# Kernel optimization log

Measured on AMD Instinct MI355X. Metric: run time of the kernel, lower is better.

Reference implementation:

```python
import jax, jax.numpy as jnp
import numpy as np

E = 1024      # embedding_size
H = 16        # num_heads
D = E // H    # head dim


def setup_inputs() -> dict:
    key = jax.random.key(0)
    k1, k2, k3, k4, k5 = jax.random.split(key, 5)
    x = jax.random.normal(k1, (4, 2048, E), dtype=jnp.float32)
    # nn.Linear(E, 3E): weight [3E, E], bias [3E]
    w_qkv = jax.random.normal(k2, (3 * E, E), dtype=jnp.float32) * (1.0 / np.sqrt(E))
    b_qkv = jax.random.normal(k3, (3 * E,), dtype=jnp.float32) * 0.02
    # nn.Linear(E, E)
    w_proj = jax.random.normal(k4, (E, E), dtype=jnp.float32) * (1.0 / np.sqrt(E))
    b_proj = jax.random.normal(k5, (E,), dtype=jnp.float32) * 0.02
    return {"x": x, "w_qkv": w_qkv, "b_qkv": b_qkv, "w_proj": w_proj, "b_proj": b_proj}


def reference(x, w_qkv, b_qkv, w_proj, b_proj):
    b, n, _ = x.shape
    qkv = x @ w_qkv.T + b_qkv                       # [b, n, 3E]
    # rearrange 'b n (h d qkv) -> qkv b h n d' : last dim grouped as (h, d, 3)
    qkv = qkv.reshape(b, n, H, D, 3)
    qkv = jnp.transpose(qkv, (4, 0, 2, 1, 3))        # [3, b, h, n, d]
    q, k, v = qkv[0], qkv[1], qkv[2]
    scale = 1.0 / np.sqrt(E / H)
    energy = jnp.einsum('bhqd,bhkd->bhqk', q, k) * scale
    attn = jax.nn.softmax(energy, axis=-1)
    out = jnp.einsum('bhqk,bhkd->bhqd', attn, v)     # [b, h, n, d]
    out = jnp.transpose(out, (0, 2, 1, 3)).reshape(b, n, E)
    return out @ w_proj.T + b_proj
```

## Files before the change

### kernel.cpp

```cpp
#include <hip/hip_runtime.h>
#include <hip/hip_fp16.h>

namespace {

constexpr int B = 4;
constexpr int N = 2048;
constexpr int E = 1024;
constexpr int H = 16;
constexpr int D = 64;
constexpr int M = B * N;

typedef __attribute__((ext_vector_type(8))) short bf16x8;
typedef __attribute__((ext_vector_type(8))) _Float16 f16x8;
typedef __attribute__((ext_vector_type(4))) float f32x4;

__device__ inline ushort bf16_rne(float f) {
  unsigned u = __float_as_uint(f);
  return (ushort)((u + 0x7FFFu + ((u >> 16) & 1u)) >> 16);
}
__device__ inline void split2(float f, ushort& hi, ushort& lo) {
  unsigned u = __float_as_uint(f);
  hi = (ushort)(u >> 16);
  lo = bf16_rne(f - __uint_as_float(u & 0xFFFF0000u));
}

__global__ __launch_bounds__(256) void split_kernel(
    const float* __restrict__ in, ushort* __restrict__ hi,
    ushort* __restrict__ lo, int n4) {
  int i = blockIdx.x * blockDim.x + threadIdx.x;
  const int stride = gridDim.x * blockDim.x;
  for (; i < n4; i += stride) {
    const float4 f = ((const float4*)in)[i];
    ushort4 h, l;
    split2(f.x, h.x, l.x);
    split2(f.y, h.y, l.y);
    split2(f.z, h.z, l.z);
    split2(f.w, h.w, l.w);
    ((ushort4*)hi)[i] = h;
    ((ushort4*)lo)[i] = l;
  }
}

template <int MODE>
__global__ __launch_bounds__(256) void gemm_x3(
    const ushort* __restrict__ Ahg, const ushort* __restrict__ Alg,
    const ushort* __restrict__ Bhg, const ushort* __restrict__ Blg,
    const float* __restrict__ bias, ushort* __restrict__ qh,
    ushort* __restrict__ ql, ushort* __restrict__ kh, ushort* __restrict__ kl,
    ushort* __restrict__ vt, float* __restrict__ outp) {
  __shared__ ushort LAh[4096], LAl[4096], LBh[4096], LBl[4096];
  const int tid = threadIdx.x;
  const int l = tid & 63, wid = tid >> 6;
  const int wr = wid >> 1, wc = wid & 1;
  const int lr = l & 15, kg = l >> 4;
  const int m0 = blockIdx.x * 128, n0 = blockIdx.y * 128;

  f32x4 acc[4][4];
#pragma unroll
  for (int i = 0; i < 4; ++i)
#pragma unroll
    for (int j = 0; j < 4; ++j) acc[i][j] = (f32x4){0.f, 0.f, 0.f, 0.f};

  for (int k0 = 0; k0 < E; k0 += 32) {
    const ushort* gAh = Ahg + (size_t)m0 * E + k0;
    const ushort* gAl = Alg + (size_t)m0 * E + k0;
    const ushort* gBh = Bhg + (size_t)n0 * E + k0;
    const ushort* gBl = Blg + (size_t)n0 * E + k0;
    __syncthreads();
    auto stage = [&](const ushort* gp, ushort* lp, int half) {
      const int c = half * 256 + tid;
      __builtin_amdgcn_global_load_lds(
          (__attribute__((address_space(1))) void*)(gp + (size_t)(c >> 2) * E +
                                                    (c & 3) * 8),
          (__attribute__((address_space(3))) void*)(lp +
                                                    (half * 256 + (tid & ~63)) * 8),
          16, 0, 0);
    };
    stage(gAh, LAh, 0); stage(gAh, LAh, 1);
    stage(gAl, LAl, 0); stage(gAl, LAl, 1);
    stage(gBh, LBh, 0); stage(gBh, LBh, 1);
    stage(gBl, LBl, 0); stage(gBl, LBl, 1);
    __syncthreads();

    bf16x8 aH[4], aL[4], bH[4], bL[4];
#pragma unroll
    for (int rb = 0; rb < 4; ++rb) {
      const int off = (wr * 64 + rb * 16 + lr) * 32 + kg * 8;
      aH[rb] = *(const bf16x8*)(LAh + off);
      aL[rb] = *(const bf16x8*)(LAl + off);
    }
#pragma unroll
    for (int cb = 0; cb < 4; ++cb) {
      const int off = (wc * 64 + cb * 16 + lr) * 32 + kg * 8;
      bH[cb] = *(const bf16x8*)(LBh + off);
      bL[cb] = *(const bf16x8*)(LBl + off);
    }
#pragma unroll
    for (int rb = 0; rb < 4; ++rb)
#pragma unroll
      for (int cb = 0; cb < 4; ++cb) {
        acc[rb][cb] = __builtin_amdgcn_mfma_f32_16x16x32_bf16(
            aH[rb], bH[cb], acc[rb][cb], 0, 0, 0);
        acc[rb][cb] = __builtin_amdgcn_mfma_f32_16x16x32_bf16(
            aH[rb], bL[cb], acc[rb][cb], 0, 0, 0);
        acc[rb][cb] = __builtin_amdgcn_mfma_f32_16x16x32_bf16(
            aL[rb], bH[cb], acc[rb][cb], 0, 0, 0);
      }
  }

#pragma unroll
  for (int cb = 0; cb < 4; ++cb) {
    const int col = n0 + wc * 64 + cb * 16 + lr;
    const float bv = bias[col];
    if (MODE == 0) {
      const int h = col / 192;
      const int rem = col - h * 192;
      const int dd = rem / 3;
      const int s = rem - dd * 3;
#pragma unroll
      for (int rb = 0; rb < 4; ++rb)
#pragma unroll
        for (int r = 0; r < 4; ++r) {
          const int m = m0 + wr * 64 + rb * 16 + kg * 4 + r;
          const int bb = m >> 11, nn = m & (N - 1);
          float v = acc[rb][cb][r] + bv;
          if (s == 0) {
            v *= 0.125f;
            ushort hi, lo;
            split2(v, hi, lo);
            const size_t idx = (((size_t)bb * H + h) * N + nn) * D + dd;
            qh[idx] = hi; ql[idx] = lo;
          } else if (s == 1) {
            ushort hi, lo;
            split2(v, hi, lo);
            const size_t idx = (((size_t)bb * H + h) * N + nn) * D + dd;
            kh[idx] = hi; kl[idx] = lo;
          } else {
            ((_Float16*)vt)[(((size_t)bb * H + h) * D + dd) * N + nn] =
                (_Float16)v;
          }
        }
    } else {
#pragma unroll
      for (int rb = 0; rb < 4; ++rb)
#pragma unroll
        for (int r = 0; r < 4; ++r) {
          const int m = m0 + wr * 64 + rb * 16 + kg * 4 + r;
          outp[(size_t)m * E + col] = acc[rb][cb][r] + bv;
        }
    }
  }
}

__global__ __launch_bounds__(256, 2) void attn_mfma(
    const ushort* __restrict__ Qh, const ushort* __restrict__ Ql,
    const ushort* __restrict__ Kh, const ushort* __restrict__ Kl,
    const ushort* __restrict__ Vt, ushort* __restrict__ Aoh,
    ushort* __restrict__ Aol) {
  __shared__ ushort KhL[4096], KlL[4096], VtL[4096], PsL[4][4096];
  const int tid = threadIdx.x;
  const int l = tid & 63, w = tid >> 6;
  const int lr = l & 15, g = l >> 4;
  const int bh = blockIdx.x, bb = bh >> 4, hh = bh & 15;
  const int q0 = blockIdx.y * 256 + w * 64;

  bf16x8 qfh[4][2], qfl[4][2];
#pragma unroll
  for (int rb = 0; rb < 4; ++rb)
#pragma unroll
    for (int ks = 0; ks < 2; ++ks) {
      const size_t off =
          ((size_t)bh * N + q0 + rb * 16 + lr) * D + ks * 32 + g * 8;
      qfh[rb][ks] = *(const bf16x8*)(Qh + off);
      qfl[rb][ks] = *(const bf16x8*)(Ql + off);
    }

  f32x4 o[4][4];
  float m_[4][4], l_[4][4];
#pragma unroll
  for (int rb = 0; rb < 4; ++rb)
#pragma unroll
    for (int r = 0; r < 4; ++r) {
      m_[rb][r] = -1e30f;
      l_[rb][r] = 0.f;
      o[rb][r] = (f32x4){0.f, 0.f, 0.f, 0.f};
    }

  ushort* Pw = &PsL[w][0];

  for (int kt = 0; kt < N / 64; ++kt) {
    __syncthreads();
#pragma unroll
    for (int bch = 0; bch < 2; ++bch) {
      const int s = bch * 256 + tid;
      const int r = s >> 3, c = s & 7;
      const int cc = (c ^ (r & 7)) * 8;
      const int dst = (bch * 256 + (tid & ~63)) * 8;
      const size_t ko = ((size_t)bh * N + kt * 64 + r) * D + cc;
      const size_t vo = ((size_t)bh * D + r) * N + kt * 64 + cc;
      __builtin_amdgcn_global_load_lds(
          (__attribute__((address_space(1))) void*)(Kh + ko),
          (__attribute__((address_space(3))) void*)(KhL + dst), 16, 0, 0);
      __builtin_amdgcn_global_load_lds(
          (__attribute__((address_space(1))) void*)(Kl + ko),
          (__attribute__((address_space(3))) void*)(KlL + dst), 16, 0, 0);
      __builtin_amdgcn_global_load_lds(
          (__attribute__((address_space(1))) void*)(Vt + vo),
          (__attribute__((address_space(3))) void*)(VtL + dst), 16, 0, 0);
    }
    __syncthreads();

    f32x4 s4[4][4];
#pragma unroll
    for (int rb = 0; rb < 4; ++rb)
#pragma unroll
      for (int cb = 0; cb < 4; ++cb) s4[rb][cb] = (f32x4){0.f, 0.f, 0.f, 0.f};
#pragma unroll
    for (int ks = 0; ks < 2; ++ks) {
      bf16x8 kfh[4], kfl[4];
#pragma unroll
      for (int cb = 0; cb < 4; ++cb) {
        const int sl = (cb * 16 + lr) * 8 + ((ks * 4 + g) ^ (lr & 7));
        kfh[cb] = *(const bf16x8*)(KhL + sl * 8);
        kfl[cb] = *(const bf16x8*)(KlL + sl * 8);
      }
#pragma unroll
      for (int rb = 0; rb < 4; ++rb)
#pragma unroll
        for (int cb = 0; cb < 4; ++cb) {
          s4[rb][cb] = __builtin_amdgcn_mfma_f32_16x16x32_bf16(
              qfh[rb][ks], kfh[cb], s4[rb][cb], 0, 0, 0);
          s4[rb][cb] = __builtin_amdgcn_mfma_f32_16x16x32_bf16(
              qfh[rb][ks], kfl[cb], s4[rb][cb], 0, 0, 0);
          s4[rb][cb] = __builtin_amdgcn_mfma_f32_16x16x32_bf16(
              qfl[rb][ks], kfh[cb], s4[rb][cb], 0, 0, 0);
        }
    }

#pragma unroll
    for (int rb = 0; rb < 4; ++rb)
#pragma unroll
      for (int r = 0; r < 4; ++r) {
        float mx = fmaxf(fmaxf(s4[rb][0][r], s4[rb][1][r]),
                         fmaxf(s4[rb][2][r], s4[rb][3][r]));
        mx = fmaxf(mx, __shfl_xor(mx, 1, 16));
        mx = fmaxf(mx, __shfl_xor(mx, 2, 16));
        mx = fmaxf(mx, __shfl_xor(mx, 4, 16));
        mx = fmaxf(mx, __shfl_xor(mx, 8, 16));
        const float mn = fmaxf(m_[rb][r], mx);
        const float fac = __expf(m_[rb][r] - mn);
        m_[rb][r] = mn;
        float sum = 0.f;
#pragma unroll
        for (int cb = 0; cb < 4; ++cb) {
          const float p = __expf(s4[rb][cb][r] - mn);
          s4[rb][cb][r] = p;
          sum += p;
        }
        sum += __shfl_xor(sum, 1, 16);
        sum += __shfl_xor(sum, 2, 16);
        sum += __shfl_xor(sum, 4, 16);
        sum += __shfl_xor(sum, 8, 16);
        l_[rb][r] = l_[rb][r] * fac + sum;
#pragma unroll
        for (int cb = 0; cb < 4; ++cb) o[rb][cb][r] *= fac;
        const int row = rb * 16 + g * 4 + r;
#pragma unroll
        for (int cb = 0; cb < 4; ++cb) {
          const int idx = (row * 64 + cb * 16 + lr) ^ ((row & 7) << 3);
          ((_Float16*)Pw)[idx] = (_Float16)s4[rb][cb][r];
        }
      }

#pragma unroll
    for (int ks = 0; ks < 2; ++ks) {
      f16x8 pf[4], vf[4];
#pragma unroll
      for (int rb = 0; rb < 4; ++rb) {
        const int sl = (rb * 16 + lr) * 8 + ((ks * 4 + g) ^ (lr & 7));
        pf[rb] = *(const f16x8*)(Pw + sl * 8);
      }
#pragma unroll
      for (int cb = 0; cb < 4; ++cb) {
        const int sl = (cb * 16 + lr) * 8 + ((ks * 4 + g) ^ (lr & 7));
        vf[cb] = *(const f16x8*)(VtL + sl * 8);
      }
#pragma unroll
      for (int rb = 0; rb < 4; ++rb)
#pragma unroll
        for (int cb = 0; cb < 4; ++cb)
          o[rb][cb] = __builtin_amdgcn_mfma_f32_16x16x32_f16(
              pf[rb], vf[cb], o[rb][cb], 0, 0, 0);
    }
  }

#pragma unroll
  for (int rb = 0; rb < 4; ++rb)
#pragma unroll
    for (int r = 0; r < 4; ++r) {
      const float inv = 1.f / l_[rb][r];
      const int n = q0 + rb * 16 + g * 4 + r;
      const size_t base = ((size_t)bb * N + n) * E + hh * D;
#pragma unroll
      for (int cb = 0; cb < 4; ++cb) {
        ushort hi, lo;
        split2(o[rb][cb][r] * inv, hi, lo);
        Aoh[base + cb * 16 + lr] = hi;
        Aol[base + cb * 16 + lr] = lo;
      }
    }
}

}

extern "C" void kernel_launch(void* const* d_in, const int* in_sizes, int n_in,
                              void* d_out, int out_size, void* d_ws,
                              size_t ws_size, hipStream_t stream) {
  (void)in_sizes; (void)n_in; (void)out_size; (void)ws_size;
  const float* x      = (const float*)d_in[0];
  const float* w_qkv  = (const float*)d_in[1];
  const float* b_qkv  = (const float*)d_in[2];
  const float* w_proj = (const float*)d_in[3];
  const float* b_proj = (const float*)d_in[4];
  float* out = (float*)d_out;

  constexpr size_t MB = 1ull << 20;
  char* w = (char*)d_ws;
  ushort* xh  = (ushort*)(w + 0 * MB);
  ushort* xl  = (ushort*)(w + 16 * MB);
  ushort* wqh = (ushort*)(w + 32 * MB);
  ushort* wql = (ushort*)(w + 38 * MB);
  ushort* wph = (ushort*)(w + 44 * MB);
  ushort* wpl = (ushort*)(w + 46 * MB);
  ushort* Aoh = (ushort*)(w + 48 * MB);
  ushort* Aol = (ushort*)(w + 64 * MB);
  ushort* Qh  = (ushort*)(w + 80 * MB);
  ushort* Ql  = (ushort*)(w + 96 * MB);
  ushort* Kh  = (ushort*)(w + 112 * MB);
  ushort* Kl  = (ushort*)(w + 128 * MB);
  ushort* Vt  = (ushort*)(w + 144 * MB);

  split_kernel<<<2048, 256, 0, stream>>>(x, xh, xl, (M * E) / 4);
  split_kernel<<<1024, 256, 0, stream>>>(w_qkv, wqh, wql, (3 * E * E) / 4);
  split_kernel<<<512, 256, 0, stream>>>(w_proj, wph, wpl, (E * E) / 4);

  gemm_x3<0><<<dim3(M / 128, 3 * E / 128), 256, 0, stream>>>(
      xh, xl, wqh, wql, b_qkv, Qh, Ql, Kh, Kl, Vt, nullptr);

  attn_mfma<<<dim3(B * H, N / 256), 256, 0, stream>>>(Qh, Ql, Kh, Kl, Vt, Aoh,
                                                      Aol);

  gemm_x3<1><<<dim3(M / 128, E / 128), 256, 0, stream>>>(
      Aoh, Aol, wph, wpl, b_proj, nullptr, nullptr, nullptr, nullptr, nullptr,
      out);
}
```

Measured before the change: 1.128 ms.

## Double-buffer attention K/V tiles, remap grid, and vectorize V-transpose stores

The attention kernel now double-buffers the K-hi, K-lo and V tiles in LDS. It prefetches the next key tile with direct global-to-LDS loads while computing on the current one, using manual vmcnt waits and barriers, and raises wave priority around the MFMA sections. The launch becomes a 1-D grid with a remapped block-to-head order, intended to improve L2 locality across XCDs. The QKV GEMM epilogue writes the transposed V as packed 4-wide fp16 stores instead of scalar stores. The extra LDS buffers increase shared memory use, which may reduce occupancy.

```diff
diff --git a/kernel.cpp b/kernel.cpp
--- a/kernel.cpp
+++ b/kernel.cpp
@@ -12,6 +12,7 @@
 
 typedef __attribute__((ext_vector_type(8))) short bf16x8;
 typedef __attribute__((ext_vector_type(8))) _Float16 f16x8;
+typedef __attribute__((ext_vector_type(4))) _Float16 f16x4;
 typedef __attribute__((ext_vector_type(4))) float f32x4;
 
 __device__ inline ushort bf16_rne(float f) {
@@ -117,29 +118,38 @@
       const int rem = col - h * 192;
       const int dd = rem / 3;
       const int s = rem - dd * 3;
-#pragma unroll
-      for (int rb = 0; rb < 4; ++rb)
-#pragma unroll
-        for (int r = 0; r < 4; ++r) {
-          const int m = m0 + wr * 64 + rb * 16 + kg * 4 + r;
+      if (s == 2) {
+#pragma unroll
+        for (int rb = 0; rb < 4; ++rb) {
+          const int m = m0 + wr * 64 + rb * 16 + kg * 4;
           const int bb = m >> 11, nn = m & (N - 1);
-          float v = acc[rb][cb][r] + bv;
-          if (s == 0) {
-            v *= 0.125f;
+          f16x4 pk;
+#pragma unroll
+          for (int r = 0; r < 4; ++r)
+            pk[r] = (_Float16)(acc[rb][cb][r] + bv);
+          *(f16x4*)((_Float16*)vt + (((size_t)bb * H + h) * D + dd) * N + nn) =
+              pk;
+        }
+      } else {
+#pragma unroll
+        for (int rb = 0; rb < 4; ++rb)
+#pragma unroll
+          for (int r = 0; r < 4; ++r) {
+            const int m = m0 + wr * 64 + rb * 16 + kg * 4 + r;
+            const int bb = m >> 11, nn = m & (N - 1);
+            float v = acc[rb][cb][r] + bv;
             ushort hi, lo;
-            split2(v, hi, lo);
             const size_t idx = (((size_t)bb * H + h) * N + nn) * D + dd;
-            qh[idx] = hi; ql[idx] = lo;
-          } else if (s == 1) {
-            ushort hi, lo;
-            split2(v, hi, lo);
-            const size_t idx = (((size_t)bb * H + h) * N + nn) * D + dd;
-            kh[idx] = hi; kl[idx] = lo;
-          } else {
-            ((_Float16*)vt)[(((size_t)bb * H + h) * D + dd) * N + nn] =
-                (_Float16)v;
+            if (s == 0) {
+              v *= 0.125f;
+              split2(v, hi, lo);
+              qh[idx] = hi; ql[idx] = lo;
+            } else {
+              split2(v, hi, lo);
+              kh[idx] = hi; kl[idx] = lo;
+            }
           }
-        }
+      }
     } else {
 #pragma unroll
       for (int rb = 0; rb < 4; ++rb)
@@ -157,12 +167,15 @@
     const ushort* __restrict__ Kh, const ushort* __restrict__ Kl,
     const ushort* __restrict__ Vt, ushort* __restrict__ Aoh,
     ushort* __restrict__ Aol) {
-  __shared__ ushort KhL[4096], KlL[4096], VtL[4096], PsL[4][4096];
+  __shared__ ushort KhL[2][4096], KlL[2][4096], VtL[2][4096], PsL[4][4096];
   const int tid = threadIdx.x;
   const int l = tid & 63, w = tid >> 6;
   const int lr = l & 15, g = l >> 4;
-  const int bh = blockIdx.x, bb = bh >> 4, hh = bh & 15;
-  const int q0 = blockIdx.y * 256 + w * 64;
+  const int id = blockIdx.x;
+  const int bh = (id & 7) * 8 + ((id >> 3) & 7);
+  const int qt = id >> 6;
+  const int bb = bh >> 4, hh = bh & 15;
+  const int q0 = qt * 256 + w * 64;
 
   bf16x8 qfh[4][2], qfl[4][2];
 #pragma unroll
@@ -188,41 +201,58 @@
 
   ushort* Pw = &PsL[w][0];
 
-  for (int kt = 0; kt < N / 64; ++kt) {
-    __syncthreads();
+  auto stage = [&](int buf, int kt) {
 #pragma unroll
     for (int bch = 0; bch < 2; ++bch) {
       const int s = bch * 256 + tid;
       const int r = s >> 3, c = s & 7;
       const int cc = (c ^ (r & 7)) * 8;
-      const int dst = (bch * 256 + (tid & ~63)) * 8;
+      const int dst = buf * 4096 + (bch * 256 + (tid & ~63)) * 8;
       const size_t ko = ((size_t)bh * N + kt * 64 + r) * D + cc;
       const size_t vo = ((size_t)bh * D + r) * N + kt * 64 + cc;
       __builtin_amdgcn_global_load_lds(
           (__attribute__((address_space(1))) void*)(Kh + ko),
-          (__attribute__((address_space(3))) void*)(KhL + dst), 16, 0, 0);
+          (__attribute__((address_space(3))) void*)(&KhL[0][0] + dst), 16, 0, 0);
       __builtin_amdgcn_global_load_lds(
           (__attribute__((address_space(1))) void*)(Kl + ko),
-          (__attribute__((address_space(3))) void*)(KlL + dst), 16, 0, 0);
+          (__attribute__((address_space(3))) void*)(&KlL[0][0] + dst), 16, 0, 0);
       __builtin_amdgcn_global_load_lds(
           (__attribute__((address_space(1))) void*)(Vt + vo),
-          (__attribute__((address_space(3))) void*)(VtL + dst), 16, 0, 0);
-    }
-    __syncthreads();
+          (__attribute__((address_space(3))) void*)(&VtL[0][0] + dst), 16, 0, 0);
+    }
+  };
+
+  constexpr int NT = N / 64;
+  stage(0, 0);
+  int cur = 0;
+
+  for (int kt = 0; kt < NT; ++kt) {
+    if (kt + 1 < NT) {
+      stage(cur ^ 1, kt + 1);
+      asm volatile("s_waitcnt vmcnt(6)" ::: "memory");
+    } else {
+      asm volatile("s_waitcnt vmcnt(0)" ::: "memory");
+    }
+    __builtin_amdgcn_s_barrier();
+
+    const ushort* KhC = &KhL[cur][0];
+    const ushort* KlC = &KlL[cur][0];
+    const ushort* VtC = &VtL[cur][0];
 
     f32x4 s4[4][4];
 #pragma unroll
     for (int rb = 0; rb < 4; ++rb)
 #pragma unroll
       for (int cb = 0; cb < 4; ++cb) s4[rb][cb] = (f32x4){0.f, 0.f, 0.f, 0.f};
+    __builtin_amdgcn_s_setprio(1);
 #pragma unroll
     for (int ks = 0; ks < 2; ++ks) {
       bf16x8 kfh[4], kfl[4];
 #pragma unroll
       for (int cb = 0; cb < 4; ++cb) {
         const int sl = (cb * 16 + lr) * 8 + ((ks * 4 + g) ^ (lr & 7));
-        kfh[cb] = *(const bf16x8*)(KhL + sl * 8);
-        kfl[cb] = *(const bf16x8*)(KlL + sl * 8);
+        kfh[cb] = *(const bf16x8*)(KhC + sl * 8);
+        kfl[cb] = *(const bf16x8*)(KlC + sl * 8);
       }
 #pragma unroll
       for (int rb = 0; rb < 4; ++rb)
@@ -236,6 +266,7 @@
               qfl[rb][ks], kfh[cb], s4[rb][cb], 0, 0, 0);
         }
     }
+    __builtin_amdgcn_s_setprio(0);
 
 #pragma unroll
     for (int rb = 0; rb < 4; ++rb)
@@ -272,6 +303,7 @@
         }
       }
 
+    __builtin_amdgcn_s_setprio(1);
 #pragma unroll
     for (int ks = 0; ks < 2; ++ks) {
       f16x8 pf[4], vf[4];
@@ -283,7 +315,7 @@
 #pragma unroll
       for (int cb = 0; cb < 4; ++cb) {
         const int sl = (cb * 16 + lr) * 8 + ((ks * 4 + g) ^ (lr & 7));
-        vf[cb] = *(const f16x8*)(VtL + sl * 8);
+        vf[cb] = *(const f16x8*)(VtC + sl * 8);
       }
 #pragma unroll
       for (int rb = 0; rb < 4; ++rb)
@@ -292,6 +324,10 @@
           o[rb][cb] = __builtin_amdgcn_mfma_f32_16x16x32_f16(
               pf[rb], vf[cb], o[rb][cb], 0, 0, 0);
     }
+    __builtin_amdgcn_s_setprio(0);
+
+    __builtin_amdgcn_s_barrier();
+    cur ^= 1;
   }
 
 #pragma unroll
@@ -347,8 +383,8 @@
   gemm_x3<0><<<dim3(M / 128, 3 * E / 128), 256, 0, stream>>>(
       xh, xl, wqh, wql, b_qkv, Qh, Ql, Kh, Kl, Vt, nullptr);
 
-  attn_mfma<<<dim3(B * H, N / 256), 256, 0, stream>>>(Qh, Ql, Kh, Kl, Vt, Aoh,
-                                                      Aol);
+  attn_mfma<<<dim3(B * H * (N / 256)), 256, 0, stream>>>(Qh, Ql, Kh, Kl, Vt,
+                                                         Aoh, Aol);
 
   gemm_x3<1><<<dim3(M / 128, E / 128), 256, 0, stream>>>(
       Aoh, Aol, wph, wpl, b_proj, nullptr, nullptr, nullptr, nullptr, nullptr,
```

Measured after the change: 1.153 ms. 2.2% more time.
